# Optimization experiments

Measured on AMD Instinct MI355X. Metric: run time of the kernel, lower is better.

Reference implementation:

```python
import jax, jax.numpy as jnp
from jax import lax
import numpy as np

H = 256  # hidden_size


def gru_last(x, Wih, Whh, bih, bhh):
    """Single-layer torch-convention GRU; returns last hidden state.
    x: [B, T, C] -> [B, H]"""
    B, T, _ = x.shape
    h_dim = Whh.shape[1]
    xW = x @ Wih.T + bih  # [B, T, 3H], precompute input gates
    def step(h, xw):
        gi_r, gi_z, gi_n = jnp.split(xw, 3, axis=-1)
        gh = h @ Whh.T + bhh
        gh_r, gh_z, gh_n = jnp.split(gh, 3, axis=-1)
        r = jax.nn.sigmoid(gi_r + gh_r)
        z = jax.nn.sigmoid(gi_z + gh_z)
        n = jnp.tanh(gi_n + r * gh_n)
        return (1.0 - z) * n + z * h, None
    h0 = jnp.zeros((B, h_dim), x.dtype)
    hT, _ = lax.scan(step, h0, jnp.swapaxes(xW, 0, 1))
    return hT


def setup_inputs() -> dict:
    key = jax.random.key(0)
    ks = jax.random.split(key, 16)
    B, N, M, C, C1 = 32, 64, 64, 64, 16
    inter = 2 * H + 6 * C + C1  # 912
    s = 0.05
    x1 = jax.random.normal(ks[0], (B, N, C1), jnp.float32)
    states = jax.random.normal(ks[1], (B, N, M, C), jnp.float32)
    perm1 = jax.vmap(lambda k: jax.random.permutation(k, M))(jax.random.split(ks[2], N)).astype(jnp.int64)
    perm2 = jax.vmap(lambda k: jax.random.permutation(k, N))(jax.random.split(ks[3], N)).astype(jnp.int64)
    return {
        "x1": x1, "states": states, "perm1": perm1, "perm2": perm2,
        # shared 2D->1D GRU (ModuleList([gru]*2) shares parameters)
        "gru2d_Wih": jax.random.normal(ks[4], (3 * H, C), jnp.float32) * s,
        "gru2d_Whh": jax.random.normal(ks[5], (3 * H, H), jnp.float32) * s,
        "gru2d_bih": jax.random.normal(ks[6], (3 * H,), jnp.float32) * s,
        "gru2d_bhh": jax.random.normal(ks[7], (3 * H,), jnp.float32) * s,
        "gru1d_Wih": jax.random.normal(ks[8], (3 * H, inter), jnp.float32) * s,
        "gru1d_Whh": jax.random.normal(ks[9], (3 * H, H), jnp.float32) * s,
        "gru1d_bih": jax.random.normal(ks[10], (3 * H,), jnp.float32) * s,
        "gru1d_bhh": jax.random.normal(ks[11], (3 * H,), jnp.float32) * s,
        "fc1_W": jax.random.normal(ks[12], (H, 3 * inter + H), jnp.float32) * s,
        "fc1_b": jax.random.normal(ks[13], (H,), jnp.float32) * s,
        "fc2_W": jax.random.normal(ks[14], (1, H), jnp.float32) * s,
        "fc2_b": jax.random.normal(ks[15], (1,), jnp.float32) * s,
    }


def reference(x1, states, perm1, perm2,
              gru2d_Wih, gru2d_Whh, gru2d_bih, gru2d_bhh,
              gru1d_Wih, gru1d_Whh, gru1d_bih, gru1d_bhh,
              fc1_W, fc1_b, fc2_W, fc2_b):
    B, N, M, C = states.shape
    d = [states.max(1), states.mean(1), states.min(1),   # [B, M, C] each (N==M)
         states.max(2), states.mean(2), states.min(2)]   # [B, N, C] each
    idx = jnp.arange(N)[:, None]
    # g1[b,i,t,c] = states[b, i, perm1[i,t], c]
    g1 = states[:, idx, perm1, :]                         # [B, N, M, C]
    # g2[b,i,t,c] = states[b, perm2[i,t], i, c]
    g2 = states[:, perm2, idx, :]                         # [B, N, N, C]
    sd1 = gru_last(g1.reshape(B * N, M, C), gru2d_Wih, gru2d_Whh, gru2d_bih, gru2d_bhh).reshape(B, N, H)
    sd2 = gru_last(g2.reshape(B * N, N, C), gru2d_Wih, gru2d_Whh, gru2d_bih, gru2d_bhh).reshape(B, N, H)
    f = jnp.concatenate(d + [sd1, sd2], axis=2)           # [B, N, 6C + 2H]
    f = jnp.concatenate([x1, f], axis=-1)                 # [B, N, inter]
    hlast = gru_last(f, gru1d_Wih, gru1d_Whh, gru1d_bih, gru1d_bhh)  # [B, H]
    g = jnp.concatenate([f.max(1), f.mean(1), f.min(1), hlast], axis=1)
    h = jax.nn.relu(g @ fc1_W.T + fc1_b)
    out = h @ fc2_W.T + fc2_b
    return out.reshape(B)
```

## Files before the change

### kernel.cpp

```cpp
#include <hip/hip_runtime.h>
#include <cmath>

#define B_ 32
#define N_ 64
#define H_ 256
#define G3_ 768
#define INTER_ 912
#define KP_ 928
#define FCIN_ 2992
#define GRED_ 2736

#define PADA 264
#define PADX 72

typedef __attribute__((ext_vector_type(8))) short short8;
typedef __attribute__((ext_vector_type(4))) short sshort4;
typedef __attribute__((ext_vector_type(4))) float float4v;

#define MFMA __builtin_amdgcn_mfma_f32_16x16x32_bf16

__device__ __forceinline__ float sigmoid_f(float x) {
    return __builtin_amdgcn_rcpf(1.0f + __builtin_amdgcn_exp2f(-1.44269504f * x));
}
__device__ __forceinline__ float tanh_fast(float x) {
    return 1.0f - 2.0f * __builtin_amdgcn_rcpf(1.0f + __builtin_amdgcn_exp2f(2.88539008f * x));
}
__device__ __forceinline__ unsigned f2bf_bits(float x) {
    unsigned u = __float_as_uint(x);
    return (u + 0x7fffu + ((u >> 16) & 1u)) >> 16;
}
__device__ __forceinline__ short f2bf(float x) { return (short)f2bf_bits(x); }

__global__ __launch_bounds__(256) void prep_kernel(
        const float* __restrict__ Whh2, const float* __restrict__ Wih2,
        const float* __restrict__ Whh1, const float* __restrict__ Wih1,
        const float* __restrict__ fc1W,
        short* __restrict__ Bfrag, short* __restrict__ Bfrag1,
        short* __restrict__ Bfrag1W, float* __restrict__ fc1Wt) {
    int idx = blockIdx.x * 256 + threadIdx.x;
    if (idx < 10 * 48 * 64 * 8) {
        int j = idx & 7, lane = (idx >> 3) & 63, tile = idx >> 9;
        int nt = tile % 48, kt = tile / 48;
        int n = nt * 16 + (lane & 15);
        int kb = (lane >> 4) * 8 + j;
        float v = (kt < 8) ? Whh2[n * 256 + kt * 32 + kb]
                           : Wih2[n * 64 + (kt - 8) * 32 + kb];
        Bfrag[idx] = f2bf(v);
    }
    if (idx < 8 * 48 * 64 * 8) {
        int j = idx & 7, lane = (idx >> 3) & 63, tile = idx >> 9;
        int nt = tile % 48, kt = tile / 48;
        int n = nt * 16 + (lane & 15);
        int k = kt * 32 + (lane >> 4) * 8 + j;
        Bfrag1[idx] = f2bf(Whh1[n * 256 + k]);
    }
    if (idx < 29 * 48 * 64 * 8) {
        int j = idx & 7, lane = (idx >> 3) & 63, tile = idx >> 9;
        int nt = tile % 48, kt = tile / 48;
        int n = nt * 16 + (lane & 15);
        int k = kt * 32 + (lane >> 4) * 8 + j;
        Bfrag1W[idx] = (k < INTER_) ? f2bf(Wih1[n * INTER_ + k]) : (short)0;
    }
    if (idx < FCIN_ * 256) {
        int o = idx & 255, i = idx >> 8;
        fc1Wt[idx] = fc1W[o * FCIN_ + i];
    }
}

__global__ __launch_bounds__(256) void reduce_states_kernel(
        const float* __restrict__ states, const float* __restrict__ x1,
        float* __restrict__ f) {
    const int c = threadIdx.x & 63;
    const int bj = blockIdx.x * 4 + (threadIdx.x >> 6);
    const int b = bj >> 6, j = bj & 63;
    const float* p1 = states + b * 262144 + j * 64 + c;
    const float* p2 = states + b * 262144 + j * 4096 + c;
    float mx1 = -1e30f, mn1 = 1e30f, sm1 = 0.f;
    float mx2 = -1e30f, mn2 = 1e30f, sm2 = 0.f;
    #pragma unroll 8
    for (int n = 0; n < 64; ++n) {
        float v = __builtin_nontemporal_load(p1 + n * 4096);
        mx1 = fmaxf(mx1, v); mn1 = fminf(mn1, v); sm1 += v;
    }
    #pragma unroll 8
    for (int m = 0; m < 64; ++m) {
        float v = __builtin_nontemporal_load(p2 + m * 64);
        mx2 = fmaxf(mx2, v); mn2 = fminf(mn2, v); sm2 += v;
    }
    float* fr = f + bj * INTER_;
    fr[16 + c]  = mx1;  fr[80 + c]  = sm1 * (1.f / 64.f);  fr[144 + c] = mn1;
    fr[208 + c] = mx2;  fr[272 + c] = sm2 * (1.f / 64.f);  fr[336 + c] = mn2;
    if (c < 16) fr[c] = x1[bj * 16 + c];
}

__global__ __launch_bounds__(512, 1) void gru2d_mfma(
        const float* __restrict__ states,
        const int* __restrict__ perm1, const int* __restrict__ perm2,
        const short* __restrict__ Bfrag,
        const float* __restrict__ bih, const float* __restrict__ bhh,
        float* __restrict__ f) {
    __shared__ short hA[2][16 * PADA];
    __shared__ short xA[2][16 * PADX];
    __shared__ short8 Blds[2 * 48 * 64];
    __shared__ int perms[1024];

    const int tid = threadIdx.x;
    const int lane = tid & 63;
    const int w = tid >> 6;
    const int m = lane & 15;
    const int q = lane >> 4;
    const bool sd2 = blockIdx.x >= 128;
    const int sblock = (blockIdx.x & 127) * 16;

    for (int i = tid; i < 1024; i += 512) {
        int r = i >> 6, t = i & 63;
        int qq = (sblock + r) & 63;
        perms[i] = sd2 ? perm2[qq * 64 + t] : perm1[qq * 64 + t];
    }
    for (int i = tid; i < 16 * PADA; i += 512) hA[0][i] = 0;
    {
        const uint4* src = (const uint4*)(Bfrag + 6 * 48 * 64 * 8);
        uint4* dst = (uint4*)Blds;
        #pragma unroll
        for (int rep = 0; rep < 12; ++rep)
            dst[tid + rep * 512] = src[tid + rep * 512];
    }

    const short8* Bf8 = (const short8*)Bfrag;
    short8 Bres[36];
    #pragma unroll
    for (int kt = 0; kt < 6; ++kt)
        #pragma unroll
        for (int j = 0; j < 6; ++j)
            Bres[kt * 6 + j] = Bf8[(kt * 48 + 8 * j + w) * 64 + lane];

    short8 Bx[12];
    #pragma unroll
    for (int kt = 0; kt < 2; ++kt)
        #pragma unroll
        for (int j = 0; j < 6; ++j)
            Bx[kt * 6 + j] = Bf8[((8 + kt) * 48 + 8 * j + w) * 64 + lane];

    const int u0 = 16 * w + m;
    const int u1 = 128 + u0;
    const float br0 = bih[u0] + bhh[u0],             br1 = bih[u1] + bhh[u1];
    const float bz0 = bih[256 + u0] + bhh[256 + u0], bz1 = bih[256 + u1] + bhh[256 + u1];
    const float bnx0 = bih[512 + u0], bnx1 = bih[512 + u1];
    const float bnh0 = bhh[512 + u0], bnh1 = bhh[512 + u1];

    float4v hreg0 = {0.f, 0.f, 0.f, 0.f}, hreg1 = {0.f, 0.f, 0.f, 0.f};

    {
        #pragma unroll
        for (int half = 0; half < 2; ++half) {
            int i = tid + half * 512;
            int r = i >> 6, c = i & 63;
            int s = sblock + r, b = s >> 6, qq = s & 63;
            int p = perms[r * 64 + 0];
            int src = sd2 ? ((b * 64 + p) * 64 + qq) * 64 + c
                          : ((b * 64 + qq) * 64 + p) * 64 + c;
            xA[0][r * PADX + c] = f2bf(states[src]);
        }
    }
    __syncthreads();

    for (int t = 0; t < 64; ++t) {
        const short* hAc = hA[t & 1];
        const short* xAc = xA[t & 1];

        float xg0 = 0.f, xg1 = 0.f;
        int w0 = -1, w1 = -1;
        if (t + 1 < 64) {
            #pragma unroll
            for (int half = 0; half < 2; ++half) {
                int i = tid + half * 512;
                int r = i >> 6, c = i & 63;
                int s = sblock + r, b = s >> 6, qq = s & 63;
                int p = perms[r * 64 + t + 1];
                int src = sd2 ? ((b * 64 + p) * 64 + qq) * 64 + c
                              : ((b * 64 + qq) * 64 + p) * 64 + c;
                float v = states[src];
                if (half == 0) { xg0 = v; w0 = r * PADX + c; }
                else           { xg1 = v; w1 = r * PADX + c; }
            }
        }

        float4v aR0 = {br0, br0, br0, br0},     aR1 = {br1, br1, br1, br1};
        float4v aZ0 = {bz0, bz0, bz0, bz0},     aZ1 = {bz1, bz1, bz1, bz1};
        float4v aNh0 = {bnh0, bnh0, bnh0, bnh0}, aNh1 = {bnh1, bnh1, bnh1, bnh1};
        float4v aNx0 = {bnx0, bnx0, bnx0, bnx0}, aNx1 = {bnx1, bnx1, bnx1, bnx1};

        #pragma unroll
        for (int kt = 0; kt < 6; ++kt) {
            short8 a = *(const short8*)(hAc + m * PADA + kt * 32 + q * 8);
            aR0  = MFMA(a, Bres[kt * 6 + 0], aR0, 0, 0, 0);
            aR1  = MFMA(a, Bres[kt * 6 + 1], aR1, 0, 0, 0);
            aZ0  = MFMA(a, Bres[kt * 6 + 2], aZ0, 0, 0, 0);
            aZ1  = MFMA(a, Bres[kt * 6 + 3], aZ1, 0, 0, 0);
            aNh0 = MFMA(a, Bres[kt * 6 + 4], aNh0, 0, 0, 0);
            aNh1 = MFMA(a, Bres[kt * 6 + 5], aNh1, 0, 0, 0);
        }
        #pragma unroll
        for (int kt = 0; kt < 2; ++kt) {
            short8 a = *(const short8*)(hAc + m * PADA + (6 + kt) * 32 + q * 8);
            short8 b0 = Blds[(kt * 48 + 8 * 0 + w) * 64 + lane];
            short8 b1 = Blds[(kt * 48 + 8 * 1 + w) * 64 + lane];
            short8 b2 = Blds[(kt * 48 + 8 * 2 + w) * 64 + lane];
            short8 b3 = Blds[(kt * 48 + 8 * 3 + w) * 64 + lane];
            short8 b4 = Blds[(kt * 48 + 8 * 4 + w) * 64 + lane];
            short8 b5 = Blds[(kt * 48 + 8 * 5 + w) * 64 + lane];
            aR0  = MFMA(a, b0, aR0, 0, 0, 0);
            aR1  = MFMA(a, b1, aR1, 0, 0, 0);
            aZ0  = MFMA(a, b2, aZ0, 0, 0, 0);
            aZ1  = MFMA(a, b3, aZ1, 0, 0, 0);
            aNh0 = MFMA(a, b4, aNh0, 0, 0, 0);
            aNh1 = MFMA(a, b5, aNh1, 0, 0, 0);
        }
        #pragma unroll
        for (int kt = 0; kt < 2; ++kt) {
            short8 a = *(const short8*)(xAc + m * PADX + kt * 32 + q * 8);
            aR0  = MFMA(a, Bx[kt * 6 + 0], aR0, 0, 0, 0);
            aR1  = MFMA(a, Bx[kt * 6 + 1], aR1, 0, 0, 0);
            aZ0  = MFMA(a, Bx[kt * 6 + 2], aZ0, 0, 0, 0);
            aZ1  = MFMA(a, Bx[kt * 6 + 3], aZ1, 0, 0, 0);
            aNx0 = MFMA(a, Bx[kt * 6 + 4], aNx0, 0, 0, 0);
            aNx1 = MFMA(a, Bx[kt * 6 + 5], aNx1, 0, 0, 0);
        }

        short* hAn = hA[(t + 1) & 1];
        #pragma unroll
        for (int p = 0; p < 4; ++p) {
            int row = q * 4 + p;
            float r0 = sigmoid_f(aR0[p]);
            float z0 = sigmoid_f(aZ0[p]);
            float n0 = tanh_fast(aNx0[p] + r0 * aNh0[p]);
            float h0 = n0 + z0 * (hreg0[p] - n0);
            hreg0[p] = h0;
            hAn[row * PADA + u0] = f2bf(h0);
            float r1 = sigmoid_f(aR1[p]);
            float z1 = sigmoid_f(aZ1[p]);
            float n1 = tanh_fast(aNx1[p] + r1 * aNh1[p]);
            float h1 = n1 + z1 * (hreg1[p] - n1);
            hreg1[p] = h1;
            hAn[row * PADA + u1] = f2bf(h1);
        }
        if (t + 1 < 64) {
            xA[(t + 1) & 1][w0] = f2bf(xg0);
            xA[(t + 1) & 1][w1] = f2bf(xg1);
        }
        __syncthreads();
    }

    const int off = sd2 ? 656 : 400;
    #pragma unroll
    for (int p = 0; p < 4; ++p) {
        int s = sblock + q * 4 + p;
        f[s * INTER_ + off + u0] = hreg0[p];
        f[s * INTER_ + off + u1] = hreg1[p];
    }
}

__global__ __launch_bounds__(256) void convert_f_kernel(
        const float* __restrict__ f, short* __restrict__ fbf) {
    int idx = blockIdx.x * 256 + threadIdx.x;
    int row = idx / 232;
    int c4 = (idx - row * 232) * 4;
    if (row >= 2048) return;
    sshort4 o;
    if (c4 < INTER_) {
        float4v v = *(const float4v*)(f + row * INTER_ + c4);
        o[0] = f2bf(v[0]); o[1] = f2bf(v[1]); o[2] = f2bf(v[2]); o[3] = f2bf(v[3]);
    } else {
        o[0] = 0; o[1] = 0; o[2] = 0; o[3] = 0;
    }
    *(sshort4*)(fbf + row * KP_ + c4) = o;
}

__global__ __launch_bounds__(256) void gemm_xw1_mfma(
        const short* __restrict__ fbf, const short* __restrict__ BfragW,
        const float* __restrict__ bih, float* __restrict__ xw) {
    const int tid = threadIdx.x;
    const int lane = tid & 63;
    const int w = tid >> 6;
    const int m = lane & 15;
    const int q = lane >> 4;
    const int tn = blockIdx.x;
    const int tm = blockIdx.y;
    const int rowb = tm * 64 + w * 16;
    const short8* Bf8 = (const short8*)BfragW;

    float4v acc[4];
    #pragma unroll
    for (int nn = 0; nn < 4; ++nn) {
        float b = bih[tn * 64 + nn * 16 + m];
        acc[nn][0] = b; acc[nn][1] = b; acc[nn][2] = b; acc[nn][3] = b;
    }

    const short* arow = fbf + (rowb + m) * KP_;
    short8 a_cur = *(const short8*)(arow + q * 8);
    short8 b_cur[4];
    #pragma unroll
    for (int nn = 0; nn < 4; ++nn)
        b_cur[nn] = Bf8[(tn * 4 + nn) * 64 + lane];

    for (int kt = 0; kt < 29; ++kt) {
        short8 a_nxt = a_cur;
        short8 b_nxt[4];
        if (kt + 1 < 29) {
            a_nxt = *(const short8*)(arow + (kt + 1) * 32 + q * 8);
            #pragma unroll
            for (int nn = 0; nn < 4; ++nn)
                b_nxt[nn] = Bf8[((kt + 1) * 48 + tn * 4 + nn) * 64 + lane];
        }
        #pragma unroll
        for (int nn = 0; nn < 4; ++nn)
            acc[nn] = MFMA(a_cur, b_cur[nn], acc[nn], 0, 0, 0);
        a_cur = a_nxt;
        #pragma unroll
        for (int nn = 0; nn < 4; ++nn) b_cur[nn] = b_nxt[nn];
    }

    #pragma unroll
    for (int p = 0; p < 4; ++p) {
        int row = rowb + q * 4 + p;
        int seq = row >> 6, t = row & 63;
        #pragma unroll
        for (int nn = 0; nn < 4; ++nn)
            xw[(t * 32 + seq) * G3_ + tn * 64 + nn * 16 + m] = acc[nn][p];
    }
}

__global__ __launch_bounds__(512, 1) void gru1d_freduce(
        const float* __restrict__ xw, const short* __restrict__ Bfrag1,
        const float* __restrict__ bhh, float* __restrict__ hlast,
        const float* __restrict__ f, float* __restrict__ g) {
    __shared__ short hA[2][16 * PADA];
    __shared__ short8 Blds[2 * 48 * 64];

    const int tid = threadIdx.x;

    if (blockIdx.x >= 2) {
        const int b = blockIdx.x - 2;
        for (int i = tid; i < INTER_; i += 512) {
            const float* fp = f + (size_t)(b * 64) * INTER_ + i;
            float mx = -1e30f, mn = 1e30f, sm = 0.f;
            #pragma unroll 8
            for (int t = 0; t < 64; ++t) {
                float v = __builtin_nontemporal_load(fp + t * INTER_);
                mx = fmaxf(mx, v); mn = fminf(mn, v); sm += v;
            }
            g[b * GRED_ + i] = mx;
            g[b * GRED_ + INTER_ + i] = sm * (1.f / 64.f);
            g[b * GRED_ + 2 * INTER_ + i] = mn;
        }
        return;
    }

    const int lane = tid & 63;
    const int w = tid >> 6;
    const int m = lane & 15;
    const int q = lane >> 4;
    const int sblock = blockIdx.x * 16;

    for (int i = tid; i < 16 * PADA; i += 512) hA[0][i] = 0;
    {
        const uint4* src = (const uint4*)(Bfrag1 + 6 * 48 * 64 * 8);
        uint4* dst = (uint4*)Blds;
        #pragma unroll
        for (int rep = 0; rep < 12; ++rep)
            dst[tid + rep * 512] = src[tid + rep * 512];
    }
    const short8* Bf8 = (const short8*)Bfrag1;
    short8 Bres[36];
    #pragma unroll
    for (int kt = 0; kt < 6; ++kt)
        #pragma unroll
        for (int j = 0; j < 6; ++j)
            Bres[kt * 6 + j] = Bf8[(kt * 48 + 8 * j + w) * 64 + lane];

    const int u0 = 16 * w + m;
    const int u1 = 128 + u0;
    const float br0 = bhh[u0],       br1 = bhh[u1];
    const float bz0 = bhh[256 + u0], bz1 = bhh[256 + u1];
    const float bn0 = bhh[512 + u0], bn1 = bhh[512 + u1];

    float4v hreg0 = {0.f, 0.f, 0.f, 0.f}, hreg1 = {0.f, 0.f, 0.f, 0.f};
    __syncthreads();

    for (int t = 0; t < 64; ++t) {
        const short* hAc = hA[t & 1];

        float giR0[4], giR1[4], giZ0[4], giZ1[4], giN0[4], giN1[4];
        #pragma unroll
        for (int p = 0; p < 4; ++p) {
            const float* gr = xw + (size_t)(t * 32 + sblock + q * 4 + p) * G3_;
            giR0[p] = gr[u0];        giR1[p] = gr[u1];
            giZ0[p] = gr[256 + u0];  giZ1[p] = gr[256 + u1];
            giN0[p] = gr[512 + u0];  giN1[p] = gr[512 + u1];
        }

        float4v aR0 = {br0, br0, br0, br0}, aR1 = {br1, br1, br1, br1};
        float4v aZ0 = {bz0, bz0, bz0, bz0}, aZ1 = {bz1, bz1, bz1, bz1};
        float4v aN0 = {bn0, bn0, bn0, bn0}, aN1 = {bn1, bn1, bn1, bn1};

        #pragma unroll
        for (int kt = 0; kt < 6; ++kt) {
            short8 a = *(const short8*)(hAc + m * PADA + kt * 32 + q * 8);
            aR0 = MFMA(a, Bres[kt * 6 + 0], aR0, 0, 0, 0);
            aR1 = MFMA(a, Bres[kt * 6 + 1], aR1, 0, 0, 0);
            aZ0 = MFMA(a, Bres[kt * 6 + 2], aZ0, 0, 0, 0);
            aZ1 = MFMA(a, Bres[kt * 6 + 3], aZ1, 0, 0, 0);
            aN0 = MFMA(a, Bres[kt * 6 + 4], aN0, 0, 0, 0);
            aN1 = MFMA(a, Bres[kt * 6 + 5], aN1, 0, 0, 0);
        }
        #pragma unroll
        for (int kt = 0; kt < 2; ++kt) {
            short8 a = *(const short8*)(hAc + m * PADA + (6 + kt) * 32 + q * 8);
            short8 b0 = Blds[(kt * 48 + 8 * 0 + w) * 64 + lane];
            short8 b1 = Blds[(kt * 48 + 8 * 1 + w) * 64 + lane];
            short8 b2 = Blds[(kt * 48 + 8 * 2 + w) * 64 + lane];
            short8 b3 = Blds[(kt * 48 + 8 * 3 + w) * 64 + lane];
            short8 b4 = Blds[(kt * 48 + 8 * 4 + w) * 64 + lane];
            short8 b5 = Blds[(kt * 48 + 8 * 5 + w) * 64 + lane];
            aR0 = MFMA(a, b0, aR0, 0, 0, 0);
            aR1 = MFMA(a, b1, aR1, 0, 0, 0);
            aZ0 = MFMA(a, b2, aZ0, 0, 0, 0);
            aZ1 = MFMA(a, b3, aZ1, 0, 0, 0);
            aN0 = MFMA(a, b4, aN0, 0, 0, 0);
            aN1 = MFMA(a, b5, aN1, 0, 0, 0);
        }

        short* hAn = hA[(t + 1) & 1];
        #pragma unroll
        for (int p = 0; p < 4; ++p) {
            int row = q * 4 + p;
            float r0 = sigmoid_f(giR0[p] + aR0[p]);
            float z0 = sigmoid_f(giZ0[p] + aZ0[p]);
            float n0 = tanh_fast(giN0[p] + r0 * aN0[p]);
            float h0 = n0 + z0 * (hreg0[p] - n0);
            hreg0[p] = h0;
            hAn[row * PADA + u0] = f2bf(h0);
            float r1 = sigmoid_f(giR1[p] + aR1[p]);
            float z1 = sigmoid_f(giZ1[p] + aZ1[p]);
            float n1 = tanh_fast(giN1[p] + r1 * aN1[p]);
            float h1 = n1 + z1 * (hreg1[p] - n1);
            hreg1[p] = h1;
            hAn[row * PADA + u1] = f2bf(h1);
        }
        __syncthreads();
    }

    #pragma unroll
    for (int p = 0; p < 4; ++p) {
        int s = sblock + q * 4 + p;
        hlast[s * 256 + u0] = hreg0[p];
        hlast[s * 256 + u1] = hreg1[p];
    }
}

__global__ __launch_bounds__(256) void tail_fc(
        const float* __restrict__ g, const float* __restrict__ hlast,
        const float* __restrict__ fc1Wt, const float* __restrict__ fc1b,
        const float* __restrict__ fc2W, const float* __restrict__ fc2b,
        float* __restrict__ out) {
    __shared__ float g_lds[FCIN_];
    __shared__ float red[4];
    const int tid = threadIdx.x;
    const int b = blockIdx.x;
    for (int i = tid; i < GRED_; i += 256) g_lds[i] = g[b * GRED_ + i];
    g_lds[GRED_ + tid] = hlast[b * 256 + tid];
    __syncthreads();

    float a0 = 0.f, a1 = 0.f, a2 = 0.f, a3 = 0.f;
    for (int i = 0; i < FCIN_; i += 4) {
        a0 = fmaf(g_lds[i],     fc1Wt[(i) * 256 + tid],     a0);
        a1 = fmaf(g_lds[i + 1], fc1Wt[(i + 1) * 256 + tid], a1);
        a2 = fmaf(g_lds[i + 2], fc1Wt[(i + 2) * 256 + tid], a2);
        a3 = fmaf(g_lds[i + 3], fc1Wt[(i + 3) * 256 + tid], a3);
    }
    float acc = ((a0 + a1) + (a2 + a3)) + fc1b[tid];
    float hv = fmaxf(acc, 0.f);
    float part = hv * fc2W[tid];
    #pragma unroll
    for (int off = 32; off >= 1; off >>= 1)
        part += __shfl_down(part, off, 64);
    if ((tid & 63) == 0) red[tid >> 6] = part;
    __syncthreads();
    if (tid == 0)
        out[b] = fc2b[0] + red[0] + red[1] + red[2] + red[3];
}

extern "C" void kernel_launch(void* const* d_in, const int* in_sizes, int n_in,
                              void* d_out, int out_size, void* d_ws, size_t ws_size,
                              hipStream_t stream) {
    const float* x1     = (const float*)d_in[0];
    const float* states = (const float*)d_in[1];
    const int*   perm1  = (const int*)d_in[2];
    const int*   perm2  = (const int*)d_in[3];
    const float* Wih2   = (const float*)d_in[4];
    const float* Whh2   = (const float*)d_in[5];
    const float* bih2   = (const float*)d_in[6];
    const float* bhh2   = (const float*)d_in[7];
    const float* Wih1   = (const float*)d_in[8];
    const float* Whh1   = (const float*)d_in[9];
    const float* bih1   = (const float*)d_in[10];
    const float* bhh1   = (const float*)d_in[11];
    const float* fc1W   = (const float*)d_in[12];
    const float* fc1b   = (const float*)d_in[13];
    const float* fc2W   = (const float*)d_in[14];
    const float* fc2b   = (const float*)d_in[15];
    float* out = (float*)d_out;

    float* ws = (float*)d_ws;
    short* Bfrag   = (short*)ws;
    short* Bfrag1  = (short*)(ws + 122880);
    short* Bfrag1W = (short*)(ws + 122880 + 98304);
    float* fc1Wt   = ws + 577536;
    float* f       = fc1Wt + FCIN_ * 256;
    short* fbf     = (short*)(f + 2048 * INTER_);
    float* xw1     = f + 2048 * INTER_ + 950272;
    float* hlast   = xw1 + 2048 * G3_;
    float* g       = hlast + 8192;

    prep_kernel<<<dim3(2992), 256, 0, stream>>>(Whh2, Wih2, Whh1, Wih1, fc1W,
                                                Bfrag, Bfrag1, Bfrag1W, fc1Wt);
    reduce_states_kernel<<<dim3(512), 256, 0, stream>>>(states, x1, f);
    gru2d_mfma<<<dim3(256), 512, 0, stream>>>(states, perm1, perm2, Bfrag,
                                              bih2, bhh2, f);
    convert_f_kernel<<<dim3(1856), 256, 0, stream>>>(f, fbf);
    gemm_xw1_mfma<<<dim3(12, 32), 256, 0, stream>>>(fbf, Bfrag1W, bih1, xw1);
    gru1d_freduce<<<dim3(34), 512, 0, stream>>>(xw1, Bfrag1, bhh1, hlast, f, g);
    tail_fc<<<dim3(32), 256, 0, stream>>>(g, hlast, fc1Wt, fc1b, fc2W, fc2b, out);
}
```

Baseline: 637.1 us.

## Double wavefronts per GRU block, one hidden tile per wave

Both recurrent GRU kernels now launch 1024 threads (16 waves) per block instead of 512. Each wave owns a single 16-unit hidden slice with three gate accumulators, where it previously owned two slices and six. This halves per-wave MFMA work and register pressure on each serial timestep, so each step's latency should shrink. In exchange, barriers cover more waves, and the input-weight fragments for the x projection are now re-read from global memory every step instead of being held in registers.

```diff
diff --git a/kernel.cpp b/kernel.cpp
--- a/kernel.cpp
+++ b/kernel.cpp
@@ -93,7 +93,7 @@
     if (c < 16) fr[c] = x1[bj * 16 + c];
 }
 
-__global__ __launch_bounds__(512, 1) void gru2d_mfma(
+__global__ __launch_bounds__(1024, 1) void gru2d_mfma(
         const float* __restrict__ states,
         const int* __restrict__ perm1, const int* __restrict__ perm2,
         const short* __restrict__ Bfrag,
@@ -112,142 +112,101 @@
     const bool sd2 = blockIdx.x >= 128;
     const int sblock = (blockIdx.x & 127) * 16;
 
-    for (int i = tid; i < 1024; i += 512) {
-        int r = i >> 6, t = i & 63;
+    {
+        int r = tid >> 6, t = tid & 63;
         int qq = (sblock + r) & 63;
-        perms[i] = sd2 ? perm2[qq * 64 + t] : perm1[qq * 64 + t];
-    }
-    for (int i = tid; i < 16 * PADA; i += 512) hA[0][i] = 0;
+        perms[tid] = sd2 ? perm2[qq * 64 + t] : perm1[qq * 64 + t];
+    }
+    for (int i = tid; i < 16 * PADA; i += 1024) hA[0][i] = 0;
     {
         const uint4* src = (const uint4*)(Bfrag + 6 * 48 * 64 * 8);
         uint4* dst = (uint4*)Blds;
         #pragma unroll
-        for (int rep = 0; rep < 12; ++rep)
-            dst[tid + rep * 512] = src[tid + rep * 512];
+        for (int rep = 0; rep < 6; ++rep)
+            dst[tid + rep * 1024] = src[tid + rep * 1024];
     }
 
     const short8* Bf8 = (const short8*)Bfrag;
-    short8 Bres[36];
-    #pragma unroll
-    for (int kt = 0; kt < 6; ++kt)
-        #pragma unroll
-        for (int j = 0; j < 6; ++j)
-            Bres[kt * 6 + j] = Bf8[(kt * 48 + 8 * j + w) * 64 + lane];
-
-    short8 Bx[12];
-    #pragma unroll
-    for (int kt = 0; kt < 2; ++kt)
-        #pragma unroll
-        for (int j = 0; j < 6; ++j)
-            Bx[kt * 6 + j] = Bf8[((8 + kt) * 48 + 8 * j + w) * 64 + lane];
-
-    const int u0 = 16 * w + m;
-    const int u1 = 128 + u0;
-    const float br0 = bih[u0] + bhh[u0],             br1 = bih[u1] + bhh[u1];
-    const float bz0 = bih[256 + u0] + bhh[256 + u0], bz1 = bih[256 + u1] + bhh[256 + u1];
-    const float bnx0 = bih[512 + u0], bnx1 = bih[512 + u1];
-    const float bnh0 = bhh[512 + u0], bnh1 = bhh[512 + u1];
-
-    float4v hreg0 = {0.f, 0.f, 0.f, 0.f}, hreg1 = {0.f, 0.f, 0.f, 0.f};
-
-    {
-        #pragma unroll
-        for (int half = 0; half < 2; ++half) {
-            int i = tid + half * 512;
-            int r = i >> 6, c = i & 63;
-            int s = sblock + r, b = s >> 6, qq = s & 63;
-            int p = perms[r * 64 + 0];
-            int src = sd2 ? ((b * 64 + p) * 64 + qq) * 64 + c
-                          : ((b * 64 + qq) * 64 + p) * 64 + c;
-            xA[0][r * PADX + c] = f2bf(states[src]);
-        }
-    }
+    short8 Bres[18];
+    #pragma unroll
+    for (int kt = 0; kt < 6; ++kt) {
+        Bres[kt * 3 + 0] = Bf8[(kt * 48 + w) * 64 + lane];
+        Bres[kt * 3 + 1] = Bf8[(kt * 48 + 16 + w) * 64 + lane];
+        Bres[kt * 3 + 2] = Bf8[(kt * 48 + 32 + w) * 64 + lane];
+    }
+
+    const int u = 16 * w + m;
+    const float br = bih[u] + bhh[u];
+    const float bz = bih[256 + u] + bhh[256 + u];
+    const float bnx = bih[512 + u];
+    const float bnh = bhh[512 + u];
+
+    const int sg = sblock + w;
+    const int bb = sg >> 6, qq = sg & 63;
+    const float* xbase = sd2 ? states + (size_t)bb * 262144 + qq * 64 + lane
+                             : states + (size_t)(bb * 64 + qq) * 4096 + lane;
+    const int pstride = sd2 ? 4096 : 64;
+    const int xwofs = w * PADX + lane;
+
+    float4v hreg = {0.f, 0.f, 0.f, 0.f};
+
+    xA[0][xwofs] = f2bf(xbase[perms[w * 64] * pstride]);
     __syncthreads();
 
     for (int t = 0; t < 64; ++t) {
         const short* hAc = hA[t & 1];
         const short* xAc = xA[t & 1];
 
-        float xg0 = 0.f, xg1 = 0.f;
-        int w0 = -1, w1 = -1;
-        if (t + 1 < 64) {
-            #pragma unroll
-            for (int half = 0; half < 2; ++half) {
-                int i = tid + half * 512;
-                int r = i >> 6, c = i & 63;
-                int s = sblock + r, b = s >> 6, qq = s & 63;
-                int p = perms[r * 64 + t + 1];
-                int src = sd2 ? ((b * 64 + p) * 64 + qq) * 64 + c
-                              : ((b * 64 + qq) * 64 + p) * 64 + c;
-                float v = states[src];
-                if (half == 0) { xg0 = v; w0 = r * PADX + c; }
-                else           { xg1 = v; w1 = r * PADX + c; }
-            }
-        }
-
-        float4v aR0 = {br0, br0, br0, br0},     aR1 = {br1, br1, br1, br1};
-        float4v aZ0 = {bz0, bz0, bz0, bz0},     aZ1 = {bz1, bz1, bz1, bz1};
-        float4v aNh0 = {bnh0, bnh0, bnh0, bnh0}, aNh1 = {bnh1, bnh1, bnh1, bnh1};
-        float4v aNx0 = {bnx0, bnx0, bnx0, bnx0}, aNx1 = {bnx1, bnx1, bnx1, bnx1};
+        float xg = 0.f;
+        if (t + 1 < 64)
+            xg = xbase[perms[w * 64 + t + 1] * pstride];
+
+        float4v aR  = {br, br, br, br};
+        float4v aZ  = {bz, bz, bz, bz};
+        float4v aNh = {bnh, bnh, bnh, bnh};
+        float4v aNx = {bnx, bnx, bnx, bnx};
 
         #pragma unroll
         for (int kt = 0; kt < 6; ++kt) {
             short8 a = *(const short8*)(hAc + m * PADA + kt * 32 + q * 8);
-            aR0  = MFMA(a, Bres[kt * 6 + 0], aR0, 0, 0, 0);
-            aR1  = MFMA(a, Bres[kt * 6 + 1], aR1, 0, 0, 0);
-            aZ0  = MFMA(a, Bres[kt * 6 + 2], aZ0, 0, 0, 0);
-            aZ1  = MFMA(a, Bres[kt * 6 + 3], aZ1, 0, 0, 0);
-            aNh0 = MFMA(a, Bres[kt * 6 + 4], aNh0, 0, 0, 0);
-            aNh1 = MFMA(a, Bres[kt * 6 + 5], aNh1, 0, 0, 0);
+            aR  = MFMA(a, Bres[kt * 3 + 0], aR, 0, 0, 0);
+            aZ  = MFMA(a, Bres[kt * 3 + 1], aZ, 0, 0, 0);
+            aNh = MFMA(a, Bres[kt * 3 + 2], aNh, 0, 0, 0);
         }
         #pragma unroll
         for (int kt = 0; kt < 2; ++kt) {
             short8 a = *(const short8*)(hAc + m * PADA + (6 + kt) * 32 + q * 8);
-            short8 b0 = Blds[(kt * 48 + 8 * 0 + w) * 64 + lane];
-            short8 b1 = Blds[(kt * 48 + 8 * 1 + w) * 64 + lane];
-            short8 b2 = Blds[(kt * 48 + 8 * 2 + w) * 64 + lane];
-            short8 b3 = Blds[(kt * 48 + 8 * 3 + w) * 64 + lane];
-            short8 b4 = Blds[(kt * 48 + 8 * 4 + w) * 64 + lane];
-            short8 b5 = Blds[(kt * 48 + 8 * 5 + w) * 64 + lane];
-            aR0  = MFMA(a, b0, aR0, 0, 0, 0);
-            aR1  = MFMA(a, b1, aR1, 0, 0, 0);
-            aZ0  = MFMA(a, b2, aZ0, 0, 0, 0);
-            aZ1  = MFMA(a, b3, aZ1, 0, 0, 0);
-            aNh0 = MFMA(a, b4, aNh0, 0, 0, 0);
-            aNh1 = MFMA(a, b5, aNh1, 0, 0, 0);
+            short8 b0 = Blds[(kt * 48 + w) * 64 + lane];
+            short8 b1 = Blds[(kt * 48 + 16 + w) * 64 + lane];
+            short8 b2 = Blds[(kt * 48 + 32 + w) * 64 + lane];
+            aR  = MFMA(a, b0, aR, 0, 0, 0);
+            aZ  = MFMA(a, b1, aZ, 0, 0, 0);
+            aNh = MFMA(a, b2, aNh, 0, 0, 0);
         }
         #pragma unroll
         for (int kt = 0; kt < 2; ++kt) {
             short8 a = *(const short8*)(xAc + m * PADX + kt * 32 + q * 8);
-            aR0  = MFMA(a, Bx[kt * 6 + 0], aR0, 0, 0, 0);
-            aR1  = MFMA(a, Bx[kt * 6 + 1], aR1, 0, 0, 0);
-            aZ0  = MFMA(a, Bx[kt * 6 + 2], aZ0, 0, 0, 0);
-            aZ1  = MFMA(a, Bx[kt * 6 + 3], aZ1, 0, 0, 0);
-            aNx0 = MFMA(a, Bx[kt * 6 + 4], aNx0, 0, 0, 0);
-            aNx1 = MFMA(a, Bx[kt * 6 + 5], aNx1, 0, 0, 0);
+            short8 b0 = Bf8[((8 + kt) * 48 + w) * 64 + lane];
+            short8 b1 = Bf8[((8 + kt) * 48 + 16 + w) * 64 + lane];
+            short8 b2 = Bf8[((8 + kt) * 48 + 32 + w) * 64 + lane];
+            aR  = MFMA(a, b0, aR, 0, 0, 0);
+            aZ  = MFMA(a, b1, aZ, 0, 0, 0);
+            aNx = MFMA(a, b2, aNx, 0, 0, 0);
         }
 
         short* hAn = hA[(t + 1) & 1];
         #pragma unroll
         for (int p = 0; p < 4; ++p) {
             int row = q * 4 + p;
-            float r0 = sigmoid_f(aR0[p]);
-            float z0 = sigmoid_f(aZ0[p]);
-            float n0 = tanh_fast(aNx0[p] + r0 * aNh0[p]);
-            float h0 = n0 + z0 * (hreg0[p] - n0);
-            hreg0[p] = h0;
-            hAn[row * PADA + u0] = f2bf(h0);
-            float r1 = sigmoid_f(aR1[p]);
-            float z1 = sigmoid_f(aZ1[p]);
-            float n1 = tanh_fast(aNx1[p] + r1 * aNh1[p]);
-            float h1 = n1 + z1 * (hreg1[p] - n1);
-            hreg1[p] = h1;
-            hAn[row * PADA + u1] = f2bf(h1);
-        }
-        if (t + 1 < 64) {
-            xA[(t + 1) & 1][w0] = f2bf(xg0);
-            xA[(t + 1) & 1][w1] = f2bf(xg1);
-        }
+            float r = sigmoid_f(aR[p]);
+            float z = sigmoid_f(aZ[p]);
+            float n = tanh_fast(aNx[p] + r * aNh[p]);
+            float h = n + z * (hreg[p] - n);
+            hreg[p] = h;
+            hAn[row * PADA + u] = f2bf(h);
+        }
+        if (t + 1 < 64)
+            xA[(t + 1) & 1][xwofs] = f2bf(xg);
         __syncthreads();
     }
 
@@ -255,8 +214,7 @@
     #pragma unroll
     for (int p = 0; p < 4; ++p) {
         int s = sblock + q * 4 + p;
-        f[s * INTER_ + off + u0] = hreg0[p];
-        f[s * INTER_ + off + u1] = hreg1[p];
+        f[s * INTER_ + off + u] = hreg[p];
     }
 }
 
@@ -330,7 +288,7 @@
     }
 }
 
-__global__ __launch_bounds__(512, 1) void gru1d_freduce(
+__global__ __launch_bounds__(1024, 1) void gru1d_freduce(
         const float* __restrict__ xw, const short* __restrict__ Bfrag1,
         const float* __restrict__ bhh, float* __restrict__ hlast,
         const float* __restrict__ f, float* __restrict__ g) {
@@ -341,7 +299,7 @@
 
     if (blockIdx.x >= 2) {
         const int b = blockIdx.x - 2;
-        for (int i = tid; i < INTER_; i += 512) {
+        for (int i = tid; i < INTER_; i += 1024) {
             const float* fp = f + (size_t)(b * 64) * INTER_ + i;
             float mx = -1e30f, mn = 1e30f, sm = 0.f;
             #pragma unroll 8
@@ -362,90 +320,75 @@
     const int q = lane >> 4;
     const int sblock = blockIdx.x * 16;
 
-    for (int i = tid; i < 16 * PADA; i += 512) hA[0][i] = 0;
+    for (int i = tid; i < 16 * PADA; i += 1024) hA[0][i] = 0;
     {
         const uint4* src = (const uint4*)(Bfrag1 + 6 * 48 * 64 * 8);
         uint4* dst = (uint4*)Blds;
         #pragma unroll
-        for (int rep = 0; rep < 12; ++rep)
-            dst[tid + rep * 512] = src[tid + rep * 512];
+        for (int rep = 0; rep < 6; ++rep)
+            dst[tid + rep * 1024] = src[tid + rep * 1024];
     }
     const short8* Bf8 = (const short8*)Bfrag1;
-    short8 Bres[36];
-    #pragma unroll
-    for (int kt = 0; kt < 6; ++kt)
-        #pragma unroll
-        for (int j = 0; j < 6; ++j)
-            Bres[kt * 6 + j] = Bf8[(kt * 48 + 8 * j + w) * 64 + lane];
-
-    const int u0 = 16 * w + m;
-    const int u1 = 128 + u0;
-    const float br0 = bhh[u0],       br1 = bhh[u1];
-    const float bz0 = bhh[256 + u0], bz1 = bhh[256 + u1];
-    const float bn0 = bhh[512 + u0], bn1 = bhh[512 + u1];
-
-    float4v hreg0 = {0.f, 0.f, 0.f, 0.f}, hreg1 = {0.f, 0.f, 0.f, 0.f};
+    short8 Bres[18];
+    #pragma unroll
+    for (int kt = 0; kt < 6; ++kt) {
+        Bres[kt * 3 + 0] = Bf8[(kt * 48 + w) * 64 + lane];
+        Bres[kt * 3 + 1] = Bf8[(kt * 48 + 16 + w) * 64 + lane];
+        Bres[kt * 3 + 2] = Bf8[(kt * 48 + 32 + w) * 64 + lane];
+    }
+
+    const int u = 16 * w + m;
+    const float br = bhh[u];
+    const float bz = bhh[256 + u];
+    const float bn = bhh[512 + u];
+
+    float4v hreg = {0.f, 0.f, 0.f, 0.f};
     __syncthreads();
 
     for (int t = 0; t < 64; ++t) {
         const short* hAc = hA[t & 1];
 
-        float giR0[4], giR1[4], giZ0[4], giZ1[4], giN0[4], giN1[4];
+        float giR[4], giZ[4], giN[4];
         #pragma unroll
         for (int p = 0; p < 4; ++p) {
             const float* gr = xw + (size_t)(t * 32 + sblock + q * 4 + p) * G3_;
-            giR0[p] = gr[u0];        giR1[p] = gr[u1];
-            giZ0[p] = gr[256 + u0];  giZ1[p] = gr[256 + u1];
-            giN0[p] = gr[512 + u0];  giN1[p] = gr[512 + u1];
-        }
-
-        float4v aR0 = {br0, br0, br0, br0}, aR1 = {br1, br1, br1, br1};
-        float4v aZ0 = {bz0, bz0, bz0, bz0}, aZ1 = {bz1, bz1, bz1, bz1};
-        float4v aN0 = {bn0, bn0, bn0, bn0}, aN1 = {bn1, bn1, bn1, bn1};
+            giR[p] = gr[u];
+            giZ[p] = gr[256 + u];
+            giN[p] = gr[512 + u];
+        }
+
+        float4v aR = {br, br, br, br};
+        float4v aZ = {bz, bz, bz, bz};
+        float4v aN = {bn, bn, bn, bn};
 
         #pragma unroll
         for (int kt = 0; kt < 6; ++kt) {
             short8 a = *(const short8*)(hAc + m * PADA + kt * 32 + q * 8);
-            aR0 = MFMA(a, Bres[kt * 6 + 0], aR0, 0, 0, 0);
-            aR1 = MFMA(a, Bres[kt * 6 + 1], aR1, 0, 0, 0);
-            aZ0 = MFMA(a, Bres[kt * 6 + 2], aZ0, 0, 0, 0);
-            aZ1 = MFMA(a, Bres[kt * 6 + 3], aZ1, 0, 0, 0);
-            aN0 = MFMA(a, Bres[kt * 6 + 4], aN0, 0, 0, 0);
-            aN1 = MFMA(a, Bres[kt * 6 + 5], aN1, 0, 0, 0);
+            aR = MFMA(a, Bres[kt * 3 + 0], aR, 0, 0, 0);
+            aZ = MFMA(a, Bres[kt * 3 + 1], aZ, 0, 0, 0);
+            aN = MFMA(a, Bres[kt * 3 + 2], aN, 0, 0, 0);
         }
         #pragma unroll
         for (int kt = 0; kt < 2; ++kt) {
             short8 a = *(const short8*)(hAc + m * PADA + (6 + kt) * 32 + q * 8);
-            short8 b0 = Blds[(kt * 48 + 8 * 0 + w) * 64 + lane];
-            short8 b1 = Blds[(kt * 48 + 8 * 1 + w) * 64 + lane];
-            short8 b2 = Blds[(kt * 48 + 8 * 2 + w) * 64 + lane];
-            short8 b3 = Blds[(kt * 48 + 8 * 3 + w) * 64 + lane];
-            short8 b4 = Blds[(kt * 48 + 8 * 4 + w) * 64 + lane];
-            short8 b5 = Blds[(kt * 48 + 8 * 5 + w) * 64 + lane];
-            aR0 = MFMA(a, b0, aR0, 0, 0, 0);
-            aR1 = MFMA(a, b1, aR1, 0, 0, 0);
-            aZ0 = MFMA(a, b2, aZ0, 0, 0, 0);
-            aZ1 = MFMA(a, b3, aZ1, 0, 0, 0);
-            aN0 = MFMA(a, b4, aN0, 0, 0, 0);
-            aN1 = MFMA(a, b5, aN1, 0, 0, 0);
+            short8 b0 = Blds[(kt * 48 + w) * 64 + lane];
+            short8 b1 = Blds[(kt * 48 + 16 + w) * 64 + lane];
+            short8 b2 = Blds[(kt * 48 + 32 + w) * 64 + lane];
+            aR = MFMA(a, b0, aR, 0, 0, 0);
+            aZ = MFMA(a, b1, aZ, 0, 0, 0);
+            aN = MFMA(a, b2, aN, 0, 0, 0);
         }
 
         short* hAn = hA[(t + 1) & 1];
         #pragma unroll
         for (int p = 0; p < 4; ++p) {
             int row = q * 4 + p;
-            float r0 = sigmoid_f(giR0[p] + aR0[p]);
-            float z0 = sigmoid_f(giZ0[p] + aZ0[p]);
-            float n0 = tanh_fast(giN0[p] + r0 * aN0[p]);
-            float h0 = n0 + z0 * (hreg0[p] - n0);
-            hreg0[p] = h0;
-            hAn[row * PADA + u0] = f2bf(h0);
-            float r1 = sigmoid_f(giR1[p] + aR1[p]);
-            float z1 = sigmoid_f(giZ1[p] + aZ1[p]);
-            float n1 = tanh_fast(giN1[p] + r1 * aN1[p]);
-            float h1 = n1 + z1 * (hreg1[p] - n1);
-            hreg1[p] = h1;
-            hAn[row * PADA + u1] = f2bf(h1);
+            float r = sigmoid_f(giR[p] + aR[p]);
+            float z = sigmoid_f(giZ[p] + aZ[p]);
+            float n = tanh_fast(giN[p] + r * aN[p]);
+            float h = n + z * (hreg[p] - n);
+            hreg[p] = h;
+            hAn[row * PADA + u] = f2bf(h);
         }
         __syncthreads();
     }
@@ -453,8 +396,7 @@
     #pragma unroll
     for (int p = 0; p < 4; ++p) {
         int s = sblock + q * 4 + p;
-        hlast[s * 256 + u0] = hreg0[p];
-        hlast[s * 256 + u1] = hreg1[p];
+        hlast[s * 256 + u] = hreg[p];
     }
 }
 
@@ -525,10 +467,10 @@
     prep_kernel<<<dim3(2992), 256, 0, stream>>>(Whh2, Wih2, Whh1, Wih1, fc1W,
                                                 Bfrag, Bfrag1, Bfrag1W, fc1Wt);
     reduce_states_kernel<<<dim3(512), 256, 0, stream>>>(states, x1, f);
-    gru2d_mfma<<<dim3(256), 512, 0, stream>>>(states, perm1, perm2, Bfrag,
-                                              bih2, bhh2, f);
+    gru2d_mfma<<<dim3(256), 1024, 0, stream>>>(states, perm1, perm2, Bfrag,
+                                               bih2, bhh2, f);
     convert_f_kernel<<<dim3(1856), 256, 0, stream>>>(f, fbf);
     gemm_xw1_mfma<<<dim3(12, 32), 256, 0, stream>>>(fbf, Bfrag1W, bih1, xw1);
-    gru1d_freduce<<<dim3(34), 512, 0, stream>>>(xw1, Bfrag1, bhh1, hlast, f, g);
+    gru1d_freduce<<<dim3(34), 1024, 0, stream>>>(xw1, Bfrag1, bhh1, hlast, f, g);
     tail_fc<<<dim3(32), 256, 0, stream>>>(g, hlast, fc1Wt, fc1b, fc2W, fc2b, out);
 }
```

Measured after the change: 841.3 us. 1.32x slower.
